# Performance work log

Hardware: AMD Instinct MI355X
Metric: run time of the kernel (lower is better)

The kernel has to match this reference:

```python
import jax, jax.numpy as jnp
import numpy as np

N_NODES = 50000
N_EDGES = 800000
HIDDEN = 128
N_GRAPHS = 256
N_CLASSES = 10


def setup_inputs() -> dict:
    key = jax.random.key(0)
    ks = jax.random.split(key, 9)
    x = jax.random.normal(ks[0], (N_NODES, HIDDEN), dtype=jnp.float32)
    edge_index = jax.random.randint(ks[1], (2, N_EDGES), 0, N_NODES, dtype=jnp.int64)
    batch = jnp.sort(jax.random.randint(ks[2], (N_NODES,), 0, N_GRAPHS, dtype=jnp.int64))
    s = 1.0 / np.sqrt(HIDDEN)
    W1 = jax.random.uniform(ks[3], (HIDDEN, HIDDEN), jnp.float32, -s, s)
    b1 = jax.random.uniform(ks[4], (HIDDEN,), jnp.float32, -s, s)
    W2 = jax.random.uniform(ks[5], (HIDDEN, HIDDEN), jnp.float32, -s, s)
    b2 = jax.random.uniform(ks[6], (HIDDEN,), jnp.float32, -s, s)
    Wl = jax.random.uniform(ks[7], (HIDDEN, N_CLASSES), jnp.float32, -s, s)
    bl = jax.random.uniform(ks[8], (N_CLASSES,), jnp.float32, -s, s)
    return {"x": x, "edge_index": edge_index, "batch": batch,
            "W1": W1, "b1": b1, "W2": W2, "b2": b2, "Wl": Wl, "bl": bl}


def _gin_conv(x, src, dst, W1, b1, W2, b2):
    # GINConv, eps=0: nn(x + sum_{j->i} x_j); messages flow src -> dst
    agg = jax.ops.segment_sum(x[src], dst, num_segments=N_NODES)
    h = x + agg
    h = jnp.maximum(h @ W1 + b1, 0.0) @ W2 + b2  # shared 2-layer MLP
    return h


def reference(x, edge_index, batch, W1, b1, W2, b2, Wl, bl):
    src, dst = edge_index[0], edge_index[1]
    h = jnp.maximum(_gin_conv(x, src, dst, W1, b1, W2, b2), 0.0)
    h = jnp.maximum(_gin_conv(h, src, dst, W1, b1, W2, b2), 0.0)
    h = _gin_conv(h, src, dst, W1, b1, W2, b2)
    # global mean pool over graphs
    sums = jax.ops.segment_sum(h, batch, num_segments=N_GRAPHS)
    cnt = jax.ops.segment_sum(jnp.ones((N_NODES,), h.dtype), batch, num_segments=N_GRAPHS)
    pooled = sums / jnp.maximum(cnt, 1.0)[:, None]
    # dropout is identity in eval mode
    return pooled @ Wl + bl
```

## Files before the change

### kernel.cpp

```cpp
#include <hip/hip_runtime.h>

#define N_NODES  50000
#define N_EDGES  800000
#define HIDDEN   128
#define N_GRAPHS 256
#define N_CLASSES 10
#define WLD 136
#define ZLD 136
#define E_HALF 400000
#define POISON 0xAAAAAAAAu

typedef short short8 __attribute__((ext_vector_type(8)));
typedef float floatx4 __attribute__((ext_vector_type(4)));

__device__ inline unsigned short bf16_rtne(float x) {
    unsigned u = __float_as_uint(x);
    unsigned r = ((u >> 16) & 1u) + 0x7fffu;
    return (unsigned short)((u + r) >> 16);
}

__device__ inline int lower_bound_batch(const int* __restrict__ batch, int target) {
    int lo = 0, hi = N_NODES;
    while (lo < hi) {
        int mid = (lo + hi) >> 1;
        if (batch[mid] < target) lo = mid + 1; else hi = mid;
    }
    return lo;
}

__global__ void prep_kernel(const int* __restrict__ dst, int* __restrict__ deg0, int* __restrict__ deg1,
                            int* __restrict__ epos,
                            const float* __restrict__ W1, unsigned short* __restrict__ W1b,
                            const float* __restrict__ W2, unsigned short* __restrict__ W2b,
                            const float4* __restrict__ X, uint4* __restrict__ Xb,
                            int* __restrict__ counter) {
    int b = blockIdx.x;
    if (b < 3125) {
        int e = b * 256 + threadIdx.x;
        int* degp = (e < E_HALF) ? deg0 : deg1;
        int old = atomicAdd(&degp[dst[e]], 1);
        epos[e] = (int)((unsigned)old - POISON);
    } else if (b < 3253) {
        int idx = (b - 3125) * 256 + threadIdx.x;
        if (idx == 0) counter[0] = 0;
        int which = idx >> 14, sub = idx & (HIDDEN * HIDDEN - 1);
        int k = sub >> 7, n = sub & 127;
        (which ? W2b : W1b)[n * HIDDEN + k] = bf16_rtne((which ? W2 : W1)[sub]);
    } else {
        int i = (b - 3253) * 256 + threadIdx.x;
        int n = i >> 4, c = i & 15;
        float4 a = X[(size_t)n * 32 + c * 2], v = X[(size_t)n * 32 + c * 2 + 1];
        uint4 o;
        o.x = (unsigned)bf16_rtne(a.x) | ((unsigned)bf16_rtne(a.y) << 16);
        o.y = (unsigned)bf16_rtne(a.z) | ((unsigned)bf16_rtne(a.w) << 16);
        o.z = (unsigned)bf16_rtne(v.x) | ((unsigned)bf16_rtne(v.y) << 16);
        o.w = (unsigned)bf16_rtne(v.z) | ((unsigned)bf16_rtne(v.w) << 16);
        Xb[(size_t)(c >> 2) * N_NODES * 4 + (size_t)n * 4 + (c & 3)] = o;
    }
}

__global__ void offsets_kernel(int* __restrict__ deg0, int* __restrict__ deg1,
                               int* __restrict__ row_start, int2* __restrict__ rsd,
                               int* __restrict__ counter) {
    int n = blockIdx.x * blockDim.x + threadIdx.x;
    int d0 = 0, dT = 0;
    if (n < N_NODES) {
        d0 = (int)((unsigned)deg0[n] - POISON);
        int d1 = (int)((unsigned)deg1[n] - POISON);
        dT = d0 + d1;
    }
    int lane = threadIdx.x & 63;
    int incl = dT;
    #pragma unroll
    for (int o = 1; o < 64; o <<= 1) {
        int v = __shfl_up(incl, o, 64);
        if (lane >= o) incl += v;
    }
    int excl = incl - dT;
    int total = __shfl(incl, 63, 64);
    int base = 0;
    if (lane == 0) base = atomicAdd(counter, total);
    base = __shfl(base, 0, 64);
    if (n < N_NODES) {
        int rs = base + excl;
        row_start[n] = rs;
        rsd[n] = make_int2(rs, d0);
        deg1[n] = dT;
    }
}

__global__ void place_kernel(const int* __restrict__ src, const int* __restrict__ dst,
                             const int* __restrict__ epos, const int2* __restrict__ rsd,
                             int* __restrict__ csr_src) {
    int e = blockIdx.x * blockDim.x + threadIdx.x;
    if (e >= N_EDGES) return;
    int d = dst[e];
    int2 rd = rsd[d];
    int pos = rd.x + epos[e];
    if (e >= E_HALF) pos += rd.y;
    csr_src[pos] = src[e];
}

__device__ inline void acc_bf2(unsigned d, float& f0, float& f1) {
    f0 += __uint_as_float(d << 16);
    f1 += __uint_as_float(d & 0xffff0000u);
}
__device__ inline void acc8(const uint4 v, float* a) {
    acc_bf2(v.x, a[0], a[1]); acc_bf2(v.y, a[2], a[3]);
    acc_bf2(v.z, a[4], a[5]); acc_bf2(v.w, a[6], a[7]);
}

__global__ void agg_kernel(const uint4* __restrict__ Xb, const int* __restrict__ row_start,
                           const int* __restrict__ deg, const int* __restrict__ csr_src,
                           uint4* __restrict__ Tb ) {
    int s = blockIdx.x & 3;
    int n = (blockIdx.x >> 2) * 64 + (threadIdx.x >> 2);
    int chunk = threadIdx.x & 3;
    if (n >= N_NODES) return;
    const uint4* Ts = Xb + (size_t)s * (N_NODES * 4);
    float a[8];
    #pragma unroll
    for (int j = 0; j < 8; ++j) a[j] = 0.f;
    {
        uint4 v = Ts[(size_t)n * 4 + chunk];
        acc8(v, a);
    }
    int rs = row_start[n], d = deg[n];
    int i = 0;
    for (; i + 4 <= d; i += 4) {
        int s0 = csr_src[rs + i + 0];
        int s1 = csr_src[rs + i + 1];
        int s2 = csr_src[rs + i + 2];
        int s3 = csr_src[rs + i + 3];
        uint4 v0 = Ts[(size_t)s0 * 4 + chunk];
        uint4 v1 = Ts[(size_t)s1 * 4 + chunk];
        uint4 v2 = Ts[(size_t)s2 * 4 + chunk];
        uint4 v3 = Ts[(size_t)s3 * 4 + chunk];
        acc8(v0, a); acc8(v1, a); acc8(v2, a); acc8(v3, a);
    }
    for (; i < d; ++i) {
        int s0 = csr_src[rs + i];
        uint4 v0 = Ts[(size_t)s0 * 4 + chunk];
        acc8(v0, a);
    }
    uint4 o;
    o.x = (unsigned)bf16_rtne(a[0]) | ((unsigned)bf16_rtne(a[1]) << 16);
    o.y = (unsigned)bf16_rtne(a[2]) | ((unsigned)bf16_rtne(a[3]) << 16);
    o.z = (unsigned)bf16_rtne(a[4]) | ((unsigned)bf16_rtne(a[5]) << 16);
    o.w = (unsigned)bf16_rtne(a[6]) | ((unsigned)bf16_rtne(a[7]) << 16);
    Tb[(size_t)n * 16 + s * 4 + chunk] = o;
}

__global__ __launch_bounds__(256)
void mlp2_kernel(const unsigned short* __restrict__ Ab,
                 const unsigned short* __restrict__ W1b,
                 const float* __restrict__ b1,
                 const unsigned short* __restrict__ W2b,
                 const float* __restrict__ b2,
                 unsigned short* __restrict__ Cb, int relu2,
                 const int* __restrict__ batch, float* __restrict__ pooled, int pool_mode) {
    __shared__ unsigned short W2S[HIDDEN * WLD];
    __shared__ unsigned short zS[128 * ZLD];

    int t = threadIdx.x;
    int w = t >> 6, l = t & 63;
    int lane16 = l & 15, quad = l >> 4;
    int node_base = blockIdx.x * 128;

    floatx4 acc[2][8];
    #pragma unroll
    for (int m = 0; m < 2; ++m)
        #pragma unroll
        for (int nt = 0; nt < 8; ++nt) acc[m][nt] = (floatx4){0.f, 0.f, 0.f, 0.f};

    #pragma unroll
    for (int kc = 0; kc < 4; ++kc) {
        int k0 = kc * 32 + quad * 8;
        short8 bt[8];
        #pragma unroll
        for (int nt = 0; nt < 8; ++nt) {
            int r = node_base + nt * 16 + lane16;
            if (r < N_NODES) bt[nt] = *(const short8*)(Ab + (size_t)r * HIDDEN + k0);
            else             bt[nt] = (short8){0,0,0,0,0,0,0,0};
        }
        short8 aw[2];
        #pragma unroll
        for (int m = 0; m < 2; ++m) {
            int zc = (2 * w + m) * 16 + lane16;
            aw[m] = *(const short8*)(W1b + (size_t)zc * HIDDEN + k0);
        }
        #pragma unroll
        for (int m = 0; m < 2; ++m)
            #pragma unroll
            for (int nt = 0; nt < 8; ++nt)
                acc[m][nt] = __builtin_amdgcn_mfma_f32_16x16x32_bf16(aw[m], bt[nt], acc[m][nt], 0, 0, 0);
    }

    {
        const short8* gh = (const short8*)W2b;
        short8 wreg[8];
        #pragma unroll
        for (int i = 0; i < 8; ++i) wreg[i] = gh[i * 256 + t];
        #pragma unroll
        for (int i = 0; i < 8; ++i) {
            int idx = i * 256 + t;
            int row = idx >> 4, kk = (idx & 15) * 8;
            *(short8*)(W2S + row * WLD + kk) = wreg[i];
        }
    }

    #pragma unroll
    for (int m = 0; m < 2; ++m) {
        int zc0 = (2 * w + m) * 16 + quad * 4;
        float4 bb = *(const float4*)(b1 + zc0);
        #pragma unroll
        for (int nt = 0; nt < 8; ++nt) {
            int node = nt * 16 + lane16;
            ushort4 pk;
            pk.x = bf16_rtne(fmaxf(acc[m][nt][0] + bb.x, 0.f));
            pk.y = bf16_rtne(fmaxf(acc[m][nt][1] + bb.y, 0.f));
            pk.z = bf16_rtne(fmaxf(acc[m][nt][2] + bb.z, 0.f));
            pk.w = bf16_rtne(fmaxf(acc[m][nt][3] + bb.w, 0.f));
            *(ushort4*)(zS + node * ZLD + zc0) = pk;
        }
    }
    __syncthreads();

    floatx4 acc2[2][8];
    #pragma unroll
    for (int m = 0; m < 2; ++m)
        #pragma unroll
        for (int nt = 0; nt < 8; ++nt) acc2[m][nt] = (floatx4){0.f, 0.f, 0.f, 0.f};

    #pragma unroll
    for (int kc = 0; kc < 4; ++kc) {
        int k0 = kc * 32 + quad * 8;
        short8 az[2];
        #pragma unroll
        for (int m = 0; m < 2; ++m) {
            int lr = w * 32 + m * 16 + lane16;
            az[m] = *(const short8*)(zS + lr * ZLD + k0);
        }
        short8 bh[8];
        #pragma unroll
        for (int nt = 0; nt < 8; ++nt)
            bh[nt] = *(const short8*)(W2S + (nt * 16 + lane16) * WLD + k0);
        #pragma unroll
        for (int m = 0; m < 2; ++m)
            #pragma unroll
            for (int nt = 0; nt < 8; ++nt)
                acc2[m][nt] = __builtin_amdgcn_mfma_f32_16x16x32_bf16(az[m], bh[nt], acc2[m][nt], 0, 0, 0);
    }

    if (!pool_mode) {
        __syncthreads();
        #pragma unroll
        for (int nt = 0; nt < 8; ++nt) {
            int col = nt * 16 + lane16;
            float b = b2[col];
            #pragma unroll
            for (int m = 0; m < 2; ++m) {
                #pragma unroll
                for (int reg = 0; reg < 4; ++reg) {
                    int rl = w * 32 + m * 16 + quad * 4 + reg;
                    float o = acc2[m][nt][reg] + b;
                    if (relu2) o = fmaxf(o, 0.f);
                    zS[rl * ZLD + col] = bf16_rtne(o);
                }
            }
        }
        __syncthreads();
        int rows = min(128, N_NODES - node_base);
        #pragma unroll
        for (int i = 0; i < 8; ++i) {
            int f = (i * 256 + t) * 8;
            int cb = f >> 12, rem = f & 4095;
            int r = rem >> 5, c0 = rem & 31;
            if (r < rows) {
                short8 v = *(const short8*)(zS + r * ZLD + cb * 32 + c0);
                *(short8*)(Cb + (size_t)cb * N_NODES * 32 + (size_t)(node_base + r) * 32 + c0) = v;
            }
        }
        return;
    }

    __syncthreads();
    #pragma unroll
    for (int nt = 0; nt < 8; ++nt) {
        int col = nt * 16 + lane16;
        float b = b2[col];
        #pragma unroll
        for (int m = 0; m < 2; ++m) {
            #pragma unroll
            for (int reg = 0; reg < 4; ++reg) {
                int rl = w * 32 + m * 16 + quad * 4 + reg;
                float o = acc2[m][nt][reg] + b;
                zS[rl * ZLD + col] = bf16_rtne(o);
            }
        }
    }
    __syncthreads();

    int row_end = min(node_base + 128, N_NODES);
    int g0 = batch[node_base];
    int gend = batch[row_end - 1];
    int c = t & 127, half = t >> 7;
    for (int g = g0; g <= gend; ++g) {
        int lo = (g == g0)   ? node_base : lower_bound_batch(batch, g);
        int hi = (g == gend) ? row_end   : lower_bound_batch(batch, g + 1);
        if (lo < node_base) lo = node_base;
        if (hi > row_end)   hi = row_end;
        float s = 0.f;
        for (int r = lo + half; r < hi; r += 2)
            s += __uint_as_float((unsigned)zS[(r - node_base) * ZLD + c] << 16);
        if (hi > lo) atomicAdd(&pooled[(size_t)g * HIDDEN + c], s);
    }
}

__global__ void head_kernel(const float* __restrict__ pooled, const int* __restrict__ batch,
                            const float* __restrict__ Wl, const float* __restrict__ bl,
                            float* __restrict__ out) {
    int g = blockIdx.x;
    int t = threadIdx.x;
    __shared__ int bounds[2];
    __shared__ float mean[HIDDEN];
    if (t < 2) bounds[t] = lower_bound_batch(batch, g + t);
    __syncthreads();
    float cntf = (float)(bounds[1] - bounds[0]);
    mean[t] = pooled[(size_t)g * HIDDEN + t] / fmaxf(cntf, 1.0f);
    __syncthreads();
    if (t < N_CLASSES) {
        float o = bl[t];
        #pragma unroll 8
        for (int k = 0; k < HIDDEN; ++k) o = fmaf(mean[k], Wl[k * N_CLASSES + t], o);
        out[(size_t)g * N_CLASSES + t] = o;
    }
}

extern "C" void kernel_launch(void* const* d_in, const int* in_sizes, int n_in,
                              void* d_out, int out_size, void* d_ws, size_t ws_size,
                              hipStream_t stream) {
    const float* x   = (const float*)d_in[0];
    const int*   ei  = (const int*)d_in[1];
    const int*   bat = (const int*)d_in[2];
    const float* W1  = (const float*)d_in[3];
    const float* b1  = (const float*)d_in[4];
    const float* W2  = (const float*)d_in[5];
    const float* b2  = (const float*)d_in[6];
    const float* Wl  = (const float*)d_in[7];
    const float* bl  = (const float*)d_in[8];
    float* out = (float*)d_out;

    const int* src = ei;
    const int* dst = ei + N_EDGES;

    char* w = (char*)d_ws;
    size_t off = 0;
    auto alloc = [&](size_t bytes) { void* p = w + off; off = (off + bytes + 255) & ~(size_t)255; return p; };
    unsigned short* g_bf  = (unsigned short*)alloc((size_t)N_NODES * HIDDEN * 2);
    unsigned short* t_bf  = (unsigned short*)alloc((size_t)N_NODES * HIDDEN * 2);
    float* pooled  = (float*)alloc((size_t)N_GRAPHS * HIDDEN * 4);
    int*   deg0    = (int*)  alloc((size_t)N_NODES * 4);
    int*   deg1    = (int*)  alloc((size_t)N_NODES * 4);
    int*   rowst   = (int*)  alloc((size_t)N_NODES * 4);
    int2*  rsd     = (int2*) alloc((size_t)N_NODES * 8);
    int*   epos    = (int*)  alloc((size_t)N_EDGES * 4);
    int*   csr_src = (int*)  alloc((size_t)N_EDGES * 4);
    int*   counter = (int*)  alloc(256);
    unsigned short* w1b = (unsigned short*)alloc((size_t)HIDDEN * HIDDEN * 2);
    unsigned short* w2b = (unsigned short*)alloc((size_t)HIDDEN * HIDDEN * 2);
    (void)ws_size; (void)in_sizes; (void)n_in; (void)out_size;

    prep_kernel<<<6378, 256, 0, stream>>>(dst, deg0, deg1, epos, W1, w1b, W2, w2b,
                                          (const float4*)x, (uint4*)g_bf, counter);
    offsets_kernel<<<(N_NODES + 255) / 256, 256, 0, stream>>>(deg0, deg1, rowst, rsd, counter);
    place_kernel<<<(N_EDGES + 255) / 256, 256, 0, stream>>>(src, dst, epos, rsd, csr_src);

    const int agg_grid = 4 * ((N_NODES + 63) / 64);
    const int mlp_grid = (N_NODES + 127) / 128;
    unsigned short* nus = (unsigned short*)nullptr;

    agg_kernel<<<agg_grid, 256, 0, stream>>>((const uint4*)g_bf, rowst, deg1, csr_src, (uint4*)t_bf);
    mlp2_kernel<<<mlp_grid, 256, 0, stream>>>(t_bf, w1b, b1, w2b, b2, g_bf, 1, bat, (float*)nullptr, 0);
    agg_kernel<<<agg_grid, 256, 0, stream>>>((const uint4*)g_bf, rowst, deg1, csr_src, (uint4*)t_bf);
    mlp2_kernel<<<mlp_grid, 256, 0, stream>>>(t_bf, w1b, b1, w2b, b2, g_bf, 1, bat, (float*)nullptr, 0);
    agg_kernel<<<agg_grid, 256, 0, stream>>>((const uint4*)g_bf, rowst, deg1, csr_src, (uint4*)t_bf);
    mlp2_kernel<<<mlp_grid, 256, 0, stream>>>(t_bf, w1b, b1, w2b, b2, nus, 0, bat, pooled, 1);

    head_kernel<<<N_GRAPHS, HIDDEN, 0, stream>>>(pooled, bat, Wl, bl, out);
}
```

Baseline: 305.0 us.

## Split MLP tile across 8 waves and unroll neighbor gather by eight

The fused MLP kernel now runs 512 threads (8 waves) per 128-node tile, with each wave owning one 16-column output slice instead of two. This halves the per-thread accumulator registers and is meant to raise occupancy and latency hiding, at the cost of each wave reloading the full node-tile B operands, which duplicates global and LDS reads. Separately, the aggregation kernel gains an 8-way unrolled gather loop so more neighbor loads are in flight at once, which adds register pressure.

```diff
diff --git a/kernel.cpp b/kernel.cpp
--- a/kernel.cpp
+++ b/kernel.cpp
@@ -127,6 +127,16 @@
     }
     int rs = row_start[n], d = deg[n];
     int i = 0;
+    for (; i + 8 <= d; i += 8) {
+        int sx[8];
+        #pragma unroll
+        for (int j = 0; j < 8; ++j) sx[j] = csr_src[rs + i + j];
+        uint4 v[8];
+        #pragma unroll
+        for (int j = 0; j < 8; ++j) v[j] = Ts[(size_t)sx[j] * 4 + chunk];
+        #pragma unroll
+        for (int j = 0; j < 8; ++j) acc8(v[j], a);
+    }
     for (; i + 4 <= d; i += 4) {
         int s0 = csr_src[rs + i + 0];
         int s1 = csr_src[rs + i + 1];
@@ -151,7 +161,7 @@
     Tb[(size_t)n * 16 + s * 4 + chunk] = o;
 }
 
-__global__ __launch_bounds__(256)
+__global__ __launch_bounds__(512, 4)
 void mlp2_kernel(const unsigned short* __restrict__ Ab,
                  const unsigned short* __restrict__ W1b,
                  const float* __restrict__ b1,
@@ -167,11 +177,9 @@
     int lane16 = l & 15, quad = l >> 4;
     int node_base = blockIdx.x * 128;
 
-    floatx4 acc[2][8];
-    #pragma unroll
-    for (int m = 0; m < 2; ++m)
-        #pragma unroll
-        for (int nt = 0; nt < 8; ++nt) acc[m][nt] = (floatx4){0.f, 0.f, 0.f, 0.f};
+    floatx4 acc[8];
+    #pragma unroll
+    for (int nt = 0; nt < 8; ++nt) acc[nt] = (floatx4){0.f, 0.f, 0.f, 0.f};
 
     #pragma unroll
     for (int kc = 0; kc < 4; ++kc) {
@@ -183,73 +191,60 @@
             if (r < N_NODES) bt[nt] = *(const short8*)(Ab + (size_t)r * HIDDEN + k0);
             else             bt[nt] = (short8){0,0,0,0,0,0,0,0};
         }
-        short8 aw[2];
-        #pragma unroll
-        for (int m = 0; m < 2; ++m) {
-            int zc = (2 * w + m) * 16 + lane16;
-            aw[m] = *(const short8*)(W1b + (size_t)zc * HIDDEN + k0);
-        }
-        #pragma unroll
-        for (int m = 0; m < 2; ++m)
-            #pragma unroll
-            for (int nt = 0; nt < 8; ++nt)
-                acc[m][nt] = __builtin_amdgcn_mfma_f32_16x16x32_bf16(aw[m], bt[nt], acc[m][nt], 0, 0, 0);
+        short8 aw;
+        {
+            int zc = w * 16 + lane16;
+            aw = *(const short8*)(W1b + (size_t)zc * HIDDEN + k0);
+        }
+        #pragma unroll
+        for (int nt = 0; nt < 8; ++nt)
+            acc[nt] = __builtin_amdgcn_mfma_f32_16x16x32_bf16(aw, bt[nt], acc[nt], 0, 0, 0);
     }
 
     {
         const short8* gh = (const short8*)W2b;
-        short8 wreg[8];
-        #pragma unroll
-        for (int i = 0; i < 8; ++i) wreg[i] = gh[i * 256 + t];
-        #pragma unroll
-        for (int i = 0; i < 8; ++i) {
-            int idx = i * 256 + t;
+        short8 wreg[4];
+        #pragma unroll
+        for (int i = 0; i < 4; ++i) wreg[i] = gh[i * 512 + t];
+        #pragma unroll
+        for (int i = 0; i < 4; ++i) {
+            int idx = i * 512 + t;
             int row = idx >> 4, kk = (idx & 15) * 8;
             *(short8*)(W2S + row * WLD + kk) = wreg[i];
         }
     }
 
-    #pragma unroll
-    for (int m = 0; m < 2; ++m) {
-        int zc0 = (2 * w + m) * 16 + quad * 4;
+    {
+        int zc0 = w * 16 + quad * 4;
         float4 bb = *(const float4*)(b1 + zc0);
         #pragma unroll
         for (int nt = 0; nt < 8; ++nt) {
             int node = nt * 16 + lane16;
             ushort4 pk;
-            pk.x = bf16_rtne(fmaxf(acc[m][nt][0] + bb.x, 0.f));
-            pk.y = bf16_rtne(fmaxf(acc[m][nt][1] + bb.y, 0.f));
-            pk.z = bf16_rtne(fmaxf(acc[m][nt][2] + bb.z, 0.f));
-            pk.w = bf16_rtne(fmaxf(acc[m][nt][3] + bb.w, 0.f));
+            pk.x = bf16_rtne(fmaxf(acc[nt][0] + bb.x, 0.f));
+            pk.y = bf16_rtne(fmaxf(acc[nt][1] + bb.y, 0.f));
+            pk.z = bf16_rtne(fmaxf(acc[nt][2] + bb.z, 0.f));
+            pk.w = bf16_rtne(fmaxf(acc[nt][3] + bb.w, 0.f));
             *(ushort4*)(zS + node * ZLD + zc0) = pk;
         }
     }
     __syncthreads();
 
-    floatx4 acc2[2][8];
-    #pragma unroll
-    for (int m = 0; m < 2; ++m)
-        #pragma unroll
-        for (int nt = 0; nt < 8; ++nt) acc2[m][nt] = (floatx4){0.f, 0.f, 0.f, 0.f};
+    floatx4 acc2[8];
+    #pragma unroll
+    for (int nt = 0; nt < 8; ++nt) acc2[nt] = (floatx4){0.f, 0.f, 0.f, 0.f};
 
     #pragma unroll
     for (int kc = 0; kc < 4; ++kc) {
         int k0 = kc * 32 + quad * 8;
-        short8 az[2];
-        #pragma unroll
-        for (int m = 0; m < 2; ++m) {
-            int lr = w * 32 + m * 16 + lane16;
-            az[m] = *(const short8*)(zS + lr * ZLD + k0);
-        }
+        short8 az = *(const short8*)(zS + (w * 16 + lane16) * ZLD + k0);
         short8 bh[8];
         #pragma unroll
         for (int nt = 0; nt < 8; ++nt)
             bh[nt] = *(const short8*)(W2S + (nt * 16 + lane16) * WLD + k0);
         #pragma unroll
-        for (int m = 0; m < 2; ++m)
-            #pragma unroll
-            for (int nt = 0; nt < 8; ++nt)
-                acc2[m][nt] = __builtin_amdgcn_mfma_f32_16x16x32_bf16(az[m], bh[nt], acc2[m][nt], 0, 0, 0);
+        for (int nt = 0; nt < 8; ++nt)
+            acc2[nt] = __builtin_amdgcn_mfma_f32_16x16x32_bf16(az, bh[nt], acc2[nt], 0, 0, 0);
     }
 
     if (!pool_mode) {
@@ -259,21 +254,18 @@
             int col = nt * 16 + lane16;
             float b = b2[col];
             #pragma unroll
-            for (int m = 0; m < 2; ++m) {
-                #pragma unroll
-                for (int reg = 0; reg < 4; ++reg) {
-                    int rl = w * 32 + m * 16 + quad * 4 + reg;
-                    float o = acc2[m][nt][reg] + b;
-                    if (relu2) o = fmaxf(o, 0.f);
-                    zS[rl * ZLD + col] = bf16_rtne(o);
-                }
+            for (int reg = 0; reg < 4; ++reg) {
+                int rl = w * 16 + quad * 4 + reg;
+                float o = acc2[nt][reg] + b;
+                if (relu2) o = fmaxf(o, 0.f);
+                zS[rl * ZLD + col] = bf16_rtne(o);
             }
         }
         __syncthreads();
         int rows = min(128, N_NODES - node_base);
         #pragma unroll
-        for (int i = 0; i < 8; ++i) {
-            int f = (i * 256 + t) * 8;
+        for (int i = 0; i < 4; ++i) {
+            int f = (i * 512 + t) * 8;
             int cb = f >> 12, rem = f & 4095;
             int r = rem >> 5, c0 = rem & 31;
             if (r < rows) {
@@ -290,13 +282,10 @@
         int col = nt * 16 + lane16;
         float b = b2[col];
         #pragma unroll
-        for (int m = 0; m < 2; ++m) {
-            #pragma unroll
-            for (int reg = 0; reg < 4; ++reg) {
-                int rl = w * 32 + m * 16 + quad * 4 + reg;
-                float o = acc2[m][nt][reg] + b;
-                zS[rl * ZLD + col] = bf16_rtne(o);
-            }
+        for (int reg = 0; reg < 4; ++reg) {
+            int rl = w * 16 + quad * 4 + reg;
+            float o = acc2[nt][reg] + b;
+            zS[rl * ZLD + col] = bf16_rtne(o);
         }
     }
     __syncthreads();
@@ -304,14 +293,14 @@
     int row_end = min(node_base + 128, N_NODES);
     int g0 = batch[node_base];
     int gend = batch[row_end - 1];
-    int c = t & 127, half = t >> 7;
+    int c = t & 127, part = t >> 7;
     for (int g = g0; g <= gend; ++g) {
         int lo = (g == g0)   ? node_base : lower_bound_batch(batch, g);
         int hi = (g == gend) ? row_end   : lower_bound_batch(batch, g + 1);
         if (lo < node_base) lo = node_base;
         if (hi > row_end)   hi = row_end;
         float s = 0.f;
-        for (int r = lo + half; r < hi; r += 2)
+        for (int r = lo + part; r < hi; r += 4)
             s += __uint_as_float((unsigned)zS[(r - node_base) * ZLD + c] << 16);
         if (hi > lo) atomicAdd(&pooled[(size_t)g * HIDDEN + c], s);
     }
@@ -381,11 +370,11 @@
     unsigned short* nus = (unsigned short*)nullptr;
 
     agg_kernel<<<agg_grid, 256, 0, stream>>>((const uint4*)g_bf, rowst, deg1, csr_src, (uint4*)t_bf);
-    mlp2_kernel<<<mlp_grid, 256, 0, stream>>>(t_bf, w1b, b1, w2b, b2, g_bf, 1, bat, (float*)nullptr, 0);
+    mlp2_kernel<<<mlp_grid, 512, 0, stream>>>(t_bf, w1b, b1, w2b, b2, g_bf, 1, bat, (float*)nullptr, 0);
     agg_kernel<<<agg_grid, 256, 0, stream>>>((const uint4*)g_bf, rowst, deg1, csr_src, (uint4*)t_bf);
-    mlp2_kernel<<<mlp_grid, 256, 0, stream>>>(t_bf, w1b, b1, w2b, b2, g_bf, 1, bat, (float*)nullptr, 0);
+    mlp2_kernel<<<mlp_grid, 512, 0, stream>>>(t_bf, w1b, b1, w2b, b2, g_bf, 1, bat, (float*)nullptr, 0);
     agg_kernel<<<agg_grid, 256, 0, stream>>>((const uint4*)g_bf, rowst, deg1, csr_src, (uint4*)t_bf);
-    mlp2_kernel<<<mlp_grid, 256, 0, stream>>>(t_bf, w1b, b1, w2b, b2, nus, 0, bat, pooled, 1);
+    mlp2_kernel<<<mlp_grid, 512, 0, stream>>>(t_bf, w1b, b1, w2b, b2, nus, 0, bat, pooled, 1);
 
     head_kernel<<<N_GRAPHS, HIDDEN, 0, stream>>>(pooled, bat, Wl, bl, out);
 }
```

Result: slower. 318.1 us (+4.3%).

## Stage node tile into LDS via async global_load_lds with XOR swizzle; read W2 from global

Applied to the files above, without the earlier changes.

The gather kernel now writes its bf16 output with an XOR-swizzled 16-byte chunk index. The MLP kernel copies its 128-node input tile directly into LDS using global_load_lds and reads it back with a matching swizzle, which avoids bank conflicts and per-lane global loads. The W2 LDS staging is dropped, so W2 fragments are read straight from global/L2. Launch bounds now request 2 blocks per SM. Risks: the bounds check for the last partial tile is gone (it reads past N_NODES rows), and W2 global reads may cost more than LDS reads.

```diff
diff --git a/kernel.cpp b/kernel.cpp
--- a/kernel.cpp
+++ b/kernel.cpp
@@ -5,7 +5,6 @@
 #define HIDDEN   128
 #define N_GRAPHS 256
 #define N_CLASSES 10
-#define WLD 136
 #define ZLD 136
 #define E_HALF 400000
 #define POISON 0xAAAAAAAAu
@@ -148,10 +147,11 @@
     o.y = (unsigned)bf16_rtne(a[2]) | ((unsigned)bf16_rtne(a[3]) << 16);
     o.z = (unsigned)bf16_rtne(a[4]) | ((unsigned)bf16_rtne(a[5]) << 16);
     o.w = (unsigned)bf16_rtne(a[6]) | ((unsigned)bf16_rtne(a[7]) << 16);
-    Tb[(size_t)n * 16 + s * 4 + chunk] = o;
-}
-
-__global__ __launch_bounds__(256)
+    int ci = (s * 4 + chunk) ^ (n & 7);
+    Tb[(size_t)n * 16 + ci] = o;
+}
+
+__global__ __launch_bounds__(256, 2)
 void mlp2_kernel(const unsigned short* __restrict__ Ab,
                  const unsigned short* __restrict__ W1b,
                  const float* __restrict__ b1,
@@ -159,13 +159,28 @@
                  const float* __restrict__ b2,
                  unsigned short* __restrict__ Cb, int relu2,
                  const int* __restrict__ batch, float* __restrict__ pooled, int pool_mode) {
-    __shared__ unsigned short W2S[HIDDEN * WLD];
+    __shared__ unsigned short TS[128 * HIDDEN];
     __shared__ unsigned short zS[128 * ZLD];
 
     int t = threadIdx.x;
+    int node_base = blockIdx.x * 128;
+
+    {
+        const char* gsrc = (const char*)(Ab + (size_t)node_base * HIDDEN);
+        char* ldst = (char*)TS;
+        #pragma unroll
+        for (int i = 0; i < 8; ++i) {
+            int idx = (i * 256 + t) * 16;
+            __builtin_amdgcn_global_load_lds(
+                (const __attribute__((address_space(1))) unsigned int*)(gsrc + idx),
+                (__attribute__((address_space(3))) unsigned int*)(ldst + idx),
+                16, 0, 0);
+        }
+    }
+
     int w = t >> 6, l = t & 63;
     int lane16 = l & 15, quad = l >> 4;
-    int node_base = blockIdx.x * 128;
+    __syncthreads();
 
     floatx4 acc[2][8];
     #pragma unroll
@@ -179,9 +194,9 @@
         short8 bt[8];
         #pragma unroll
         for (int nt = 0; nt < 8; ++nt) {
-            int r = node_base + nt * 16 + lane16;
-            if (r < N_NODES) bt[nt] = *(const short8*)(Ab + (size_t)r * HIDDEN + k0);
-            else             bt[nt] = (short8){0,0,0,0,0,0,0,0};
+            int row = nt * 16 + lane16;
+            int ci = (kc * 4 + quad) ^ (row & 7);
+            bt[nt] = *(const short8*)(TS + row * HIDDEN + ci * 8);
         }
         short8 aw[2];
         #pragma unroll
@@ -194,19 +209,6 @@
             #pragma unroll
             for (int nt = 0; nt < 8; ++nt)
                 acc[m][nt] = __builtin_amdgcn_mfma_f32_16x16x32_bf16(aw[m], bt[nt], acc[m][nt], 0, 0, 0);
-    }
-
-    {
-        const short8* gh = (const short8*)W2b;
-        short8 wreg[8];
-        #pragma unroll
-        for (int i = 0; i < 8; ++i) wreg[i] = gh[i * 256 + t];
-        #pragma unroll
-        for (int i = 0; i < 8; ++i) {
-            int idx = i * 256 + t;
-            int row = idx >> 4, kk = (idx & 15) * 8;
-            *(short8*)(W2S + row * WLD + kk) = wreg[i];
-        }
     }
 
     #pragma unroll
@@ -244,7 +246,7 @@
         short8 bh[8];
         #pragma unroll
         for (int nt = 0; nt < 8; ++nt)
-            bh[nt] = *(const short8*)(W2S + (nt * 16 + lane16) * WLD + k0);
+            bh[nt] = *(const short8*)(W2b + (size_t)(nt * 16 + lane16) * HIDDEN + k0);
         #pragma unroll
         for (int m = 0; m < 2; ++m)
             #pragma unroll
```

Result: no change. 302.6 us (-0.8%).
